# Performance work log

Measured on AMD Instinct MI355X. Metric: run time of the kernel, lower is better.

## Reference

```python
import jax, jax.numpy as jnp
import numpy as np

EPS = 1e-5  # torch LayerNorm default

def layer_norm(x, scale, bias):
    m = jnp.mean(x, axis=-1, keepdims=True)
    v = jnp.var(x, axis=-1, keepdims=True)
    return (x - m) * jax.lax.rsqrt(v + EPS) * scale + bias

def setup_inputs() -> dict:
    key = jax.random.key(0)
    ks = jax.random.split(key, 8)
    B, N, E, D = 2, 50000, 262144, 256
    node_features = jax.random.normal(ks[0], (B, N, D), jnp.float32)
    edge_index = jax.random.randint(ks[1], (B, E, 2), 0, N)
    edge_relations = jax.random.normal(ks[2], (B, E, D), jnp.float32)
    edge_mask = jnp.ones((B, E), jnp.float32)
    sc = 1.0 / np.sqrt(D).astype(np.float32)
    rel_w = jax.random.normal(ks[3], (D, D), jnp.float32) * sc
    rel_b = jnp.zeros((D,), jnp.float32)
    norm_s = jnp.ones((D,), jnp.float32)
    norm_b = jnp.zeros((D,), jnp.float32)
    w1 = jax.random.normal(ks[4], (D, 4 * D), jnp.float32) * sc
    b1 = jnp.zeros((4 * D,), jnp.float32)
    w2 = jax.random.normal(ks[5], (4 * D, D), jnp.float32) * (1.0 / np.sqrt(4 * D).astype(np.float32))
    b2 = jnp.zeros((D,), jnp.float32)
    ffn_s = jnp.ones((D,), jnp.float32)
    ffn_b = jnp.zeros((D,), jnp.float32)
    return dict(node_features=node_features, edge_relations=edge_relations,
                edge_mask=edge_mask, rel_w=rel_w, rel_b=rel_b,
                norm_s=norm_s, norm_b=norm_b, w1=w1, b1=b1, w2=w2, b2=b2,
                ffn_s=ffn_s, ffn_b=ffn_b, edge_index=edge_index)

def reference(node_features, edge_relations, edge_mask, rel_w, rel_b,
              norm_s, norm_b, w1, b1, w2, b2, ffn_s, ffn_b, edge_index):
    B, N, D = node_features.shape
    bidx = jnp.arange(B)[:, None]                      # [B,1] batch index for gather/scatter
    src_idx = edge_index[:, :, 0]                      # [B,E]
    tgt_idx = edge_index[:, :, 1]                      # [B,E]
    src_features = node_features[bidx, src_idx]        # gather -> [B,E,D]
    rel_features = edge_relations @ rel_w + rel_b      # [B,E,D]
    messages = (src_features + rel_features) * edge_mask[..., None]
    aggregated = jnp.zeros_like(node_features).at[bidx, tgt_idx].add(messages)
    counts = jnp.zeros((B, N, 1), node_features.dtype).at[bidx, tgt_idx].add(edge_mask[..., None])
    counts = jnp.maximum(counts, 1.0)
    aggregated = aggregated / counts
    x = layer_norm(node_features + aggregated, norm_s, norm_b)
    h = jax.nn.gelu(x @ w1 + b1, approximate=False)    # torch GELU default = exact erf
    x = layer_norm(x + (h @ w2 + b2), ffn_s, ffn_b)
    return x
```

## Files before the change

kernel.cpp:

```cpp
#include <hip/hip_runtime.h>
#include <math.h>

#define Bn 2
#define Nn 50000
#define En 262144
#define Dn 256
#define Hn 1024
#define RTOT (Bn*Nn)

typedef short bf16x8 __attribute__((ext_vector_type(8)));
typedef float f32x4 __attribute__((ext_vector_type(4)));

__device__ __forceinline__ short f2b(float f) {
  unsigned u = __float_as_uint(f);
  u = u + 0x7fffu + ((u >> 16) & 1u);
  return (short)(u >> 16);
}
__device__ __forceinline__ float b2f(unsigned short s) {
  return __uint_as_float(((unsigned)s) << 16);
}

__device__ __forceinline__ float gelu_f(float v) {
  float x = fabsf(v) * 0.70710678118654752f;
  float t = __builtin_amdgcn_rcpf(1.0f + 0.47047f * x);
  float p = t*(0.3480242f + t*(-0.0958798f + t*0.7478556f));
  float er = 1.0f - p * __expf(-x*x);
  er = copysignf(er, v);
  return 0.5f * v * (1.0f + er);
}

__device__ __forceinline__ void gl16(const void* g, void* l) {
  __builtin_amdgcn_global_load_lds(
      (const __attribute__((address_space(1))) unsigned int*)g,
      (__attribute__((address_space(3))) unsigned int*)l, 16, 0, 0);
}

__global__ void __launch_bounds__(256) wconv(
    const float* __restrict__ relw, const float* __restrict__ w1,
    const float* __restrict__ w2, short* __restrict__ relwT,
    short* __restrict__ w1s, short* __restrict__ w2s) {
  int tid = blockIdx.x * 256 + threadIdx.x;
  if (tid < Dn*Dn) { int c = tid >> 8, k = tid & 255; relwT[tid] = f2b(relw[k*Dn + c]); }
  int t1 = tid - Dn*Dn;
  if (t1 >= 0 && t1 < Dn*Hn) {
    int kk = t1 >> 16, rem = t1 & 65535;
    int col = rem >> 6, kl = rem & 63;
    w1s[kk*65536 + col*64 + (kl ^ ((col & 7) << 3))] = f2b(w1[(kk*64 + kl)*Hn + col]);
  }
  int t2 = tid - Dn*Dn - Dn*Hn;
  if (t2 >= 0 && t2 < Hn*Dn) {
    int kk = t2 >> 14, rem = t2 & 16383;
    int col = rem >> 6, kl = rem & 63;
    w2s[kk*16384 + col*64 + (kl ^ ((col & 7) << 3))] = f2b(w2[(kk*64 + kl)*Dn + col]);
  }
}

__global__ void __launch_bounds__(256) histk(const int* __restrict__ ei, int* __restrict__ cnt) {
  int tid = blockIdx.x * 256 + threadIdx.x;
  if (tid >= Bn*En) return;
  int b = tid / En;
  int tgt = ei[tid*2 + 1];
  atomicAdd(&cnt[b*Nn + tgt], 1);
}

__global__ void __launch_bounds__(256) offsk(const int* __restrict__ cnt,
                                             int* __restrict__ offs, int* __restrict__ gtot) {
  int i = blockIdx.x * 256 + threadIdx.x;
  int lane = threadIdx.x & 63;
  int v = (i < RTOT) ? cnt[i] : 0;
  int s = v;
#pragma unroll
  for (int d = 1; d < 64; d <<= 1) {
    int t = __shfl_up(s, d, 64);
    if (lane >= d) s += t;
  }
  int base = 0;
  if (lane == 63) base = atomicAdd(gtot, s);
  base = __shfl(base, 63, 64);
  if (i < RTOT) offs[i] = base + s - v;
}

__global__ void __launch_bounds__(256) fillk(const int* __restrict__ ei, const int* __restrict__ offs,
                                             int* __restrict__ cursor, int* __restrict__ eids) {
  int tid = blockIdx.x * 256 + threadIdx.x;
  if (tid >= Bn*En) return;
  int b = tid / En, e = tid - b*En;
  int tgt = ei[tid*2 + 1];
  int node = b*Nn + tgt;
  int pos = atomicAdd(&cursor[node], 1);
  eids[offs[node] + pos] = e;
}

__global__ void __launch_bounds__(256) aggk(
    const float* __restrict__ nodef, const float* __restrict__ erel,
    const float* __restrict__ emask, const int* __restrict__ ei,
    const int* __restrict__ offs, const int* __restrict__ cnt,
    const int* __restrict__ eids,
    short* __restrict__ sumrelB, short* __restrict__ sumsrcB, float* __restrict__ cntf) {
  int w = (blockIdx.x * 256 + threadIdx.x) >> 6;
  int lane = threadIdx.x & 63;
  if (w >= RTOT) return;
  int b = w / Nn;
  const size_t ebase = (size_t)b * En;
  const size_t nbase = (size_t)b * Nn;
  int s0 = offs[w], kall = cnt[w];
  int h = lane >> 5, l32 = lane & 31;
  float r[8] = {}, a[8] = {};
  float cf = 0.f;
  for (int base = 0; base < kall; base += 64) {
    int k = kall - base; if (k > 64) k = 64;
    int e = 0, sr = 0; float m = 0.f;
    if (lane < k) {
      e  = eids[s0 + base + lane];
      sr = ei[(ebase + e)*2];
      m  = emask[ebase + e];
    }
    for (int j = 0; j < k; j += 2) {
      int je = j + h;
      int e1  = __shfl(e, je, 64);
      int sr1 = __shfl(sr, je, 64);
      float m1 = __shfl(m, je, 64);
      if (je < k) {
        const float* rp = erel  + (ebase + e1)*Dn + l32*8;
        const float* np = nodef + (nbase + sr1)*Dn + l32*8;
        float4 rv0 = *(const float4*)rp;
        float4 rv1 = *(const float4*)(rp + 4);
        float4 nv0 = *(const float4*)np;
        float4 nv1 = *(const float4*)(np + 4);
        r[0]+=rv0.x*m1; r[1]+=rv0.y*m1; r[2]+=rv0.z*m1; r[3]+=rv0.w*m1;
        r[4]+=rv1.x*m1; r[5]+=rv1.y*m1; r[6]+=rv1.z*m1; r[7]+=rv1.w*m1;
        a[0]+=nv0.x*m1; a[1]+=nv0.y*m1; a[2]+=nv0.z*m1; a[3]+=nv0.w*m1;
        a[4]+=nv1.x*m1; a[5]+=nv1.y*m1; a[6]+=nv1.z*m1; a[7]+=nv1.w*m1;
        cf += m1;
      }
    }
  }
#pragma unroll
  for (int i = 0; i < 8; i++) {
    r[i] += __shfl_xor(r[i], 32, 64);
    a[i] += __shfl_xor(a[i], 32, 64);
  }
  cf += __shfl_xor(cf, 32, 64);
  bf16x8 o;
  if (h == 0) {
#pragma unroll
    for (int i = 0; i < 8; i++) o[i] = f2b(r[i]);
    *(bf16x8*)((char*)sumrelB + (size_t)w*512 + ((l32*16) ^ ((w & 7) << 4))) = o;
  } else {
#pragma unroll
    for (int i = 0; i < 8; i++) o[i] = f2b(a[i]);
    *(bf16x8*)((char*)sumsrcB + (size_t)w*512 + ((l32*16) ^ ((w & 7) << 4))) = o;
  }
  if (lane == 0) cntf[w] = cf;
}

__device__ __forceinline__ bf16x8 ldsA(const char* lds, int r, int kb) {
  int byte = r*512 + (((kb)*2) ^ ((r & 7) << 4));
  return *(const bf16x8*)(lds + byte);
}

__global__ void __launch_bounds__(256, 3) relln(
    const short* __restrict__ sumrelB, const short* __restrict__ relwT,
    const float* __restrict__ relb, const float* __restrict__ nodef,
    const short* __restrict__ sumsrcB, const float* __restrict__ cntf,
    const float* __restrict__ ns, const float* __restrict__ nb,
    short* __restrict__ xb) {
  constexpr int MR = 2;
  __shared__ __align__(16) char lds[16384 + 33280 + 1024];
  char* ldsS = lds;
  char* ldsN = lds + 16384;
  float* red = (float*)(lds + 16384 + 33280);
  int tid = threadIdx.x;
  int lane = tid & 63, wv = tid >> 6;
  int l15 = lane & 15, l4 = lane >> 4;
  int row0 = blockIdx.x * 32;
#pragma unroll
  for (int i = 0; i < 4; i++) {
    int u = tid + 256*i;
    int r = u >> 5, wb = (u & 31) * 16;
    gl16((const char*)sumrelB + (size_t)(row0 + r)*512 + wb, ldsS + u*16);
  }
#pragma unroll
  for (int i = 0; i < 8; i++) {
    int u = tid + 256*i;
    int r = u >> 6, c4 = u & 63;
    float4 v = *(const float4*)(nodef + (size_t)(row0 + r)*Dn + c4*4);
    *(float4*)(ldsN + r*1040 + c4*16) = v;
  }
  __syncthreads();
  f32x4 acc[MR][4] = {};
#pragma unroll
  for (int ks = 0; ks < 8; ks++) {
    bf16x8 af[MR], bfr[4];
#pragma unroll
    for (int m = 0; m < MR; m++) af[m] = ldsA(ldsS, m*16 + l15, ks*32 + l4*8);
#pragma unroll
    for (int n = 0; n < 4; n++) {
      int col = wv*64 + n*16 + l15;
      bfr[n] = *(const bf16x8*)(relwT + col*Dn + ks*32 + l4*8);
    }
#pragma unroll
    for (int m = 0; m < MR; m++)
#pragma unroll
      for (int n = 0; n < 4; n++)
        acc[m][n] = __builtin_amdgcn_mfma_f32_16x16x32_bf16(af[m], bfr[n], acc[m][n], 0, 0, 0);
  }
  __syncthreads();
#pragma unroll
  for (int i = 0; i < 4; i++) {
    int u = tid + 256*i;
    int r = u >> 5, wb = (u & 31) * 16;
    gl16((const char*)sumsrcB + (size_t)(row0 + r)*512 + wb, ldsS + u*16);
  }
  __syncthreads();
  int cols[4]; float rb_c[4], ns_c[4], nb_c[4];
#pragma unroll
  for (int n = 0; n < 4; n++) {
    cols[n] = wv*64 + n*16 + l15;
    rb_c[n] = relb[cols[n]]; ns_c[n] = ns[cols[n]]; nb_c[n] = nb[cols[n]];
  }
  float s1[MR][4], s2[MR][4];
#pragma unroll
  for (int m = 0; m < MR; m++)
#pragma unroll
    for (int g = 0; g < 4; g++) {
      int r = m*16 + l4*4 + g; int rg = row0 + r;
      float cf  = cntf[rg];
      float inv = 1.0f / fmaxf(cf, 1.0f);
      float aa = 0.f, qq = 0.f;
#pragma unroll
      for (int n = 0; n < 4; n++) {
        float ssrc = b2f(*(const unsigned short*)(ldsS + r*512 + ((cols[n]*2) ^ ((r & 7) << 4))));
        float nfv  = *(const float*)(ldsN + r*1040 + cols[n]*4);
        float vv = nfv + (ssrc + acc[m][n][g] + cf*rb_c[n]) * inv;
        acc[m][n][g] = vv;
        aa += vv; qq += vv*vv;
      }
#pragma unroll
      for (int d = 1; d < 16; d <<= 1) { aa += __shfl_xor(aa, d, 16); qq += __shfl_xor(qq, d, 16); }
      s1[m][g] = aa; s2[m][g] = qq;
    }
  if (l15 == 0) {
#pragma unroll
    for (int m = 0; m < MR; m++)
#pragma unroll
      for (int g = 0; g < 4; g++) {
        int r = m*16 + l4*4 + g;
        red[(wv*32 + r)*2]     = s1[m][g];
        red[(wv*32 + r)*2 + 1] = s2[m][g];
      }
  }
  __syncthreads();
#pragma unroll
  for (int m = 0; m < MR; m++)
#pragma unroll
    for (int g = 0; g < 4; g++) {
      int r = m*16 + l4*4 + g; int rg = row0 + r;
      float t1 = 0.f, t2 = 0.f;
#pragma unroll
      for (int u = 0; u < 4; u++) { t1 += red[(u*32 + r)*2]; t2 += red[(u*32 + r)*2 + 1]; }
      float mean = t1 * (1.0f/Dn);
      float var  = t2 * (1.0f/Dn) - mean*mean;
      float rstd = rsqrtf(var + 1e-5f);
#pragma unroll
      for (int n = 0; n < 4; n++) {
        float xv = (acc[m][n][g] - mean)*rstd*ns_c[n] + nb_c[n];
        *(short*)((char*)xb + (size_t)rg*512 + ((cols[n]*2) ^ ((rg & 7) << 4))) = f2b(xv);
      }
    }
}

__global__ void __launch_bounds__(256) ffn1k(
    const short* __restrict__ xb, const short* __restrict__ w1s,
    const float* __restrict__ b1, short* __restrict__ H) {
  __shared__ __align__(16) char lds[32768];
  char* Xa = lds;
  char* Wa = lds + 16384;
  int tid = threadIdx.x;
  int lane = tid & 63, wv = tid >> 6;
  int l15 = lane & 15, l4 = lane >> 4;
  int wm = wv >> 1, wn = wv & 1;
  int row0 = blockIdx.x * 128;
  int col0 = blockIdx.y * 128;

  f32x4 acc[4][4] = {};
#pragma unroll 1
  for (int kk = 0; kk < 4; kk++) {
#pragma unroll
    for (int i = 0; i < 4; i++) {
      int u = tid + 256*i;
      int r = u >> 3, wb = (u & 7) * 16;
      int gr = row0 + r; if (gr > RTOT - 1) gr = RTOT - 1;
      gl16((const char*)xb + (size_t)gr*512 + kk*128 + wb, Xa + u*16);
    }
#pragma unroll
    for (int i = 0; i < 4; i++) {
      int u = tid + 256*i;
      gl16((const char*)w1s + (size_t)kk*131072 + col0*128 + u*16, Wa + u*16);
    }
    __syncthreads();
#pragma unroll
    for (int ksl = 0; ksl < 2; ksl++) {
      int kb2 = (ksl*32 + l4*8) * 2;
      bf16x8 af[4], bw[4];
#pragma unroll
      for (int mf = 0; mf < 4; mf++) {
        int r = wm*64 + mf*16 + l15;
        af[mf] = *(const bf16x8*)(Xa + r*128 + (kb2 ^ ((r & 7) << 4)));
      }
#pragma unroll
      for (int nf = 0; nf < 4; nf++) {
        int c = wn*64 + nf*16 + l15;
        bw[nf] = *(const bf16x8*)(Wa + c*128 + (kb2 ^ ((c & 7) << 4)));
      }
#pragma unroll
      for (int mf = 0; mf < 4; mf++)
#pragma unroll
        for (int nf = 0; nf < 4; nf++)
          acc[mf][nf] = __builtin_amdgcn_mfma_f32_16x16x32_bf16(af[mf], bw[nf], acc[mf][nf], 0, 0, 0);
    }
    __syncthreads();
  }
  float b1v[4];
#pragma unroll
  for (int nf = 0; nf < 4; nf++) b1v[nf] = b1[col0 + wn*64 + nf*16 + l15];
#pragma unroll
  for (int mf = 0; mf < 4; mf++)
#pragma unroll
    for (int g = 0; g < 4; g++) {
      int R = wm*64 + mf*16 + l4*4 + g;
#pragma unroll
      for (int nf = 0; nf < 4; nf++) {
        int C = wn*64 + nf*16 + l15;
        float hv = gelu_f(acc[mf][nf][g] + b1v[nf]);
        *(short*)(lds + R*256 + ((C*2) ^ ((R & 7) << 4))) = f2b(hv);
      }
    }
  __syncthreads();
#pragma unroll
  for (int i = 0; i < 8; i++) {
    int u = tid + 256*i;
    int r = u >> 4, c = (u & 15) * 8;
    int gr = row0 + r;
    if (gr >= RTOT) continue;
    bf16x8 v = *(const bf16x8*)(lds + r*256 + ((c*2) ^ ((r & 7) << 4)));
    int gc = col0 + c;
    size_t hb = (size_t)gr*2048 + (gc >> 6)*128 + (((gc & 63)*2) ^ ((gr & 7) << 4));
    *(bf16x8*)((char*)H + hb) = v;
  }
}

__global__ void __launch_bounds__(512, 4) ffn2k(
    const short* __restrict__ H, const short* __restrict__ w2s,
    const float* __restrict__ b2, const float* __restrict__ fs,
    const float* __restrict__ fb, const short* __restrict__ xb,
    float* __restrict__ out) {
  __shared__ __align__(16) char lds[8192 + 32768];
  char* Ha  = lds;
  char* W2a = lds + 8192;
  float* red = (float*)lds;
  int tid = threadIdx.x;
  int lane = tid & 63, wv = tid >> 6;
  int l15 = lane & 15, l4 = lane >> 4;
  int wm = wv >> 2, wn = wv & 3;
  int rows0 = blockIdx.x * 64;

  f32x4 acc[2][4] = {};
#pragma unroll 1
  for (int kk = 0; kk < 16; kk++) {
    {
      int flat = wv*1024 + lane*16;
      int r = flat >> 7, bo = flat & 127;
      int lr = rows0 + r; if (lr > RTOT - 1) lr = RTOT - 1;
      gl16((const char*)H + (size_t)lr*2048 + kk*128 + bo, Ha + flat);
    }
#pragma unroll
    for (int i = 0; i < 4; i++) {
      int base = wv*4096 + i*1024;
      gl16((const char*)w2s + (size_t)kk*32768 + base + lane*16, W2a + base + lane*16);
    }
    __syncthreads();
#pragma unroll
    for (int ksl = 0; ksl < 2; ksl++) {
      bf16x8 ah[2], bw[4];
#pragma unroll
      for (int mf = 0; mf < 2; mf++) {
        int r = wm*32 + mf*16 + l15;
        ah[mf] = *(const bf16x8*)(Ha + r*128 + (((ksl*32 + l4*8)*2) ^ ((r & 7) << 4)));
      }
#pragma unroll
      for (int nf = 0; nf < 4; nf++) {
        int c = wn*64 + nf*16 + l15;
        bw[nf] = *(const bf16x8*)(W2a + c*128 + (((ksl*32 + l4*8)*2) ^ ((c & 7) << 4)));
      }
#pragma unroll
      for (int mf = 0; mf < 2; mf++)
#pragma unroll
        for (int nf = 0; nf < 4; nf++)
          acc[mf][nf] = __builtin_amdgcn_mfma_f32_16x16x32_bf16(ah[mf], bw[nf], acc[mf][nf], 0, 0, 0);
    }
    __syncthreads();
  }
#pragma unroll
  for (int i = 0; i < 4; i++) {
    int u = tid + 512*i;
    int r = u >> 5, wb = (u & 31) * 16;
    int lr = rows0 + r; if (lr > RTOT - 1) lr = RTOT - 1;
    gl16((const char*)xb + (size_t)lr*512 + wb, W2a + u*16);
  }
  __syncthreads();
  float b2c[4], fsc[4], fbc[4];
#pragma unroll
  for (int nf = 0; nf < 4; nf++) {
    int col = wn*64 + nf*16 + l15;
    b2c[nf] = b2[col]; fsc[nf] = fs[col]; fbc[nf] = fb[col];
  }
#pragma unroll
  for (int mf = 0; mf < 2; mf++)
#pragma unroll
    for (int g = 0; g < 4; g++) {
      int R = wm*32 + mf*16 + l4*4 + g;
      float a = 0.f, q = 0.f;
#pragma unroll
      for (int nf = 0; nf < 4; nf++) {
        int col = wn*64 + nf*16 + l15;
        float xv = b2f(*(const unsigned short*)(W2a + R*512 + ((col*2) ^ ((R & 7) << 4))));
        float vv = xv + acc[mf][nf][g] + b2c[nf];
        acc[mf][nf][g] = vv;
        a += vv; q += vv*vv;
      }
#pragma unroll
      for (int d = 1; d < 16; d <<= 1) { a += __shfl_xor(a, d, 16); q += __shfl_xor(q, d, 16); }
      if (l15 == 0) {
        red[(wn*64 + R)*2]     = a;
        red[(wn*64 + R)*2 + 1] = q;
      }
    }
  __syncthreads();
#pragma unroll
  for (int mf = 0; mf < 2; mf++)
#pragma unroll
    for (int g = 0; g < 4; g++) {
      int R = wm*32 + mf*16 + l4*4 + g;
      int gr = rows0 + R;
      if (gr >= RTOT) continue;
      float t1 = 0.f, t2 = 0.f;
#pragma unroll
      for (int u = 0; u < 4; u++) { t1 += red[(u*64 + R)*2]; t2 += red[(u*64 + R)*2 + 1]; }
      float mean = t1 * (1.0f/Dn);
      float var  = t2 * (1.0f/Dn) - mean*mean;
      float rstd = rsqrtf(var + 1e-5f);
#pragma unroll
      for (int nf = 0; nf < 4; nf++) {
        int col = wn*64 + nf*16 + l15;
        out[(size_t)gr*Dn + col] = (acc[mf][nf][g] - mean)*rstd*fsc[nf] + fbc[nf];
      }
    }
}

extern "C" void kernel_launch(void* const* d_in, const int* in_sizes, int n_in,
                              void* d_out, int out_size, void* d_ws, size_t ws_size,
                              hipStream_t stream) {
  const float* nodef = (const float*)d_in[0];
  const float* erel  = (const float*)d_in[1];
  const float* emask = (const float*)d_in[2];
  const float* relw  = (const float*)d_in[3];
  const float* relb  = (const float*)d_in[4];
  const float* ns    = (const float*)d_in[5];
  const float* nb    = (const float*)d_in[6];
  const float* w1    = (const float*)d_in[7];
  const float* b1    = (const float*)d_in[8];
  const float* w2    = (const float*)d_in[9];
  const float* b2    = (const float*)d_in[10];
  const float* fs    = (const float*)d_in[11];
  const float* fb    = (const float*)d_in[12];
  const int*   ei    = (const int*)d_in[13];
  float* out = (float*)d_out;
  char* ws = (char*)d_ws;

  constexpr size_t SZ_ROWB = (size_t)RTOT * Dn * 2;
  constexpr size_t O_SRB = 0;
  constexpr size_t O_SSB = O_SRB + SZ_ROWB;
  constexpr size_t O_XB  = O_SSB + SZ_ROWB;
  constexpr size_t O_H   = O_XB + SZ_ROWB;
  constexpr size_t O_CNT = O_H + (size_t)RTOT * Hn * 2;
  constexpr size_t O_CUR = O_CNT + (size_t)RTOT*4;
  constexpr size_t O_OFF = O_CUR + (size_t)RTOT*4;
  constexpr size_t O_EID = O_OFF + ((size_t)(RTOT+1)*4 + 124);
  constexpr size_t O_CNTF = O_EID + (size_t)Bn*En*4;
  constexpr size_t O_RWT = O_CNTF + (size_t)RTOT*4;
  constexpr size_t O_W1T = O_RWT + (size_t)Dn*Dn*2;
  constexpr size_t O_W2T = O_W1T + (size_t)Dn*Hn*2;
  constexpr size_t WS_NEED = O_W2T + (size_t)Hn*Dn*2;
  if (ws_size < WS_NEED) return;

  short* sumrelB = (short*)(ws + O_SRB);
  short* sumsrcB = (short*)(ws + O_SSB);
  short* xb      = (short*)(ws + O_XB);
  short* Hbuf    = (short*)(ws + O_H);
  int*   cnt    = (int*)(ws + O_CNT);
  int*   cursor = (int*)(ws + O_CUR);
  int*   offs   = (int*)(ws + O_OFF);
  int*   eids   = (int*)(ws + O_EID);
  float* cntf   = (float*)(ws + O_CNTF);
  short* relwT  = (short*)(ws + O_RWT);
  short* w1s    = (short*)(ws + O_W1T);
  short* w2s    = (short*)(ws + O_W2T);
  int*   gtot   = offs + RTOT;

  hipMemsetAsync(ws + O_CNT, 0, O_EID - O_CNT, stream);

  wconv<<<(Dn*Dn + Dn*Hn + Hn*Dn + 255) / 256, 256, 0, stream>>>(relw, w1, w2, relwT, w1s, w2s);
  histk<<<(Bn*En) / 256, 256, 0, stream>>>(ei, cnt);
  offsk<<<(RTOT + 255) / 256, 256, 0, stream>>>(cnt, offs, gtot);
  fillk<<<(Bn*En) / 256, 256, 0, stream>>>(ei, offs, cursor, eids);
  aggk<<<(RTOT + 3) / 4, 256, 0, stream>>>(nodef, erel, emask, ei, offs, cnt, eids,
                                           sumrelB, sumsrcB, cntf);
  relln<<<RTOT / 32, 256, 0, stream>>>(sumrelB, relwT, relb, nodef, sumsrcB, cntf, ns, nb, xb);
  ffn1k<<<dim3((RTOT + 127) / 128, Hn / 128), 256, 0, stream>>>(xb, w1s, b1, Hbuf);
  ffn2k<<<(RTOT + 63) / 64, 512, 0, stream>>>(Hbuf, w2s, b2, fs, fb, xb, out);
}
```

Before: 612.1 us.

## Pack edge records in CSR fill and widen per-edge gather to four edges per wave

```diff
diff --git a/kernel.cpp b/kernel.cpp
--- a/kernel.cpp
+++ b/kernel.cpp
@@ -80,22 +80,23 @@
   if (i < RTOT) offs[i] = base + s - v;
 }
 
-__global__ void __launch_bounds__(256) fillk(const int* __restrict__ ei, const int* __restrict__ offs,
-                                             int* __restrict__ cursor, int* __restrict__ eids) {
+__global__ void __launch_bounds__(256) fillk(const int* __restrict__ ei,
+                                             const float* __restrict__ emask,
+                                             int* __restrict__ offs, int4* __restrict__ erec) {
   int tid = blockIdx.x * 256 + threadIdx.x;
   if (tid >= Bn*En) return;
   int b = tid / En, e = tid - b*En;
-  int tgt = ei[tid*2 + 1];
-  int node = b*Nn + tgt;
-  int pos = atomicAdd(&cursor[node], 1);
-  eids[offs[node] + pos] = e;
+  int2 st = *(const int2*)(ei + (size_t)tid*2);
+  float m = emask[tid];
+  int node = b*Nn + st.y;
+  int pos = atomicAdd(&offs[node], 1);
+  erec[pos] = make_int4(e, st.x, __float_as_int(m), 0);
 }
 
 __global__ void __launch_bounds__(256) aggk(
     const float* __restrict__ nodef, const float* __restrict__ erel,
-    const float* __restrict__ emask, const int* __restrict__ ei,
     const int* __restrict__ offs, const int* __restrict__ cnt,
-    const int* __restrict__ eids,
+    const int4* __restrict__ erec,
     short* __restrict__ sumrelB, short* __restrict__ sumsrcB, float* __restrict__ cntf) {
   int w = (blockIdx.x * 256 + threadIdx.x) >> 6;
   int lane = threadIdx.x & 63;
@@ -103,53 +104,56 @@
   int b = w / Nn;
   const size_t ebase = (size_t)b * En;
   const size_t nbase = (size_t)b * Nn;
-  int s0 = offs[w], kall = cnt[w];
-  int h = lane >> 5, l32 = lane & 31;
-  float r[8] = {}, a[8] = {};
+  int kall = cnt[w];
+  int s0 = offs[w] - kall;
+  int g = lane >> 4, l16 = lane & 15;
+  float r[16] = {}, a[16] = {};
   float cf = 0.f;
   for (int base = 0; base < kall; base += 64) {
     int k = kall - base; if (k > 64) k = 64;
-    int e = 0, sr = 0; float m = 0.f;
-    if (lane < k) {
-      e  = eids[s0 + base + lane];
-      sr = ei[(ebase + e)*2];
-      m  = emask[ebase + e];
-    }
-    for (int j = 0; j < k; j += 2) {
-      int je = j + h;
-      int e1  = __shfl(e, je, 64);
-      int sr1 = __shfl(sr, je, 64);
-      float m1 = __shfl(m, je, 64);
+    int4 rec = make_int4(0, 0, 0, 0);
+    if (lane < k) rec = erec[s0 + base + lane];
+    for (int j = 0; j < k; j += 4) {
+      int je = j + g;
+      int e1  = __shfl(rec.x, je, 64);
+      int sr1 = __shfl(rec.y, je, 64);
+      float m1 = __int_as_float(__shfl(rec.z, je, 64));
       if (je < k) {
-        const float* rp = erel  + (ebase + e1)*Dn + l32*8;
-        const float* np = nodef + (nbase + sr1)*Dn + l32*8;
-        float4 rv0 = *(const float4*)rp;
-        float4 rv1 = *(const float4*)(rp + 4);
-        float4 nv0 = *(const float4*)np;
-        float4 nv1 = *(const float4*)(np + 4);
-        r[0]+=rv0.x*m1; r[1]+=rv0.y*m1; r[2]+=rv0.z*m1; r[3]+=rv0.w*m1;
-        r[4]+=rv1.x*m1; r[5]+=rv1.y*m1; r[6]+=rv1.z*m1; r[7]+=rv1.w*m1;
-        a[0]+=nv0.x*m1; a[1]+=nv0.y*m1; a[2]+=nv0.z*m1; a[3]+=nv0.w*m1;
-        a[4]+=nv1.x*m1; a[5]+=nv1.y*m1; a[6]+=nv1.z*m1; a[7]+=nv1.w*m1;
+        const float* rp = erel  + (ebase + e1)*Dn + l16*16;
+        const float* np = nodef + (nbase + sr1)*Dn + l16*16;
+#pragma unroll
+        for (int q = 0; q < 4; q++) {
+          float4 rv = *(const float4*)(rp + q*4);
+          float4 nv = *(const float4*)(np + q*4);
+          r[q*4+0]+=rv.x*m1; r[q*4+1]+=rv.y*m1; r[q*4+2]+=rv.z*m1; r[q*4+3]+=rv.w*m1;
+          a[q*4+0]+=nv.x*m1; a[q*4+1]+=nv.y*m1; a[q*4+2]+=nv.z*m1; a[q*4+3]+=nv.w*m1;
+        }
         cf += m1;
       }
     }
   }
 #pragma unroll
-  for (int i = 0; i < 8; i++) {
+  for (int i = 0; i < 16; i++) {
+    r[i] += __shfl_xor(r[i], 16, 64);
+    a[i] += __shfl_xor(a[i], 16, 64);
     r[i] += __shfl_xor(r[i], 32, 64);
     a[i] += __shfl_xor(a[i], 32, 64);
   }
+  cf += __shfl_xor(cf, 16, 64);
   cf += __shfl_xor(cf, 32, 64);
-  bf16x8 o;
-  if (h == 0) {
-#pragma unroll
-    for (int i = 0; i < 8; i++) o[i] = f2b(r[i]);
-    *(bf16x8*)((char*)sumrelB + (size_t)w*512 + ((l32*16) ^ ((w & 7) << 4))) = o;
-  } else {
-#pragma unroll
-    for (int i = 0; i < 8; i++) o[i] = f2b(a[i]);
-    *(bf16x8*)((char*)sumsrcB + (size_t)w*512 + ((l32*16) ^ ((w & 7) << 4))) = o;
+  int c0 = l16*32;
+  if (g == 0) {
+    bf16x8 o0, o1;
+#pragma unroll
+    for (int i = 0; i < 8; i++) { o0[i] = f2b(r[i]); o1[i] = f2b(r[i+8]); }
+    *(bf16x8*)((char*)sumrelB + (size_t)w*512 + (c0 ^ ((w & 7) << 4))) = o0;
+    *(bf16x8*)((char*)sumrelB + (size_t)w*512 + ((c0+16) ^ ((w & 7) << 4))) = o1;
+  } else if (g == 1) {
+    bf16x8 o0, o1;
+#pragma unroll
+    for (int i = 0; i < 8; i++) { o0[i] = f2b(a[i]); o1[i] = f2b(a[i+8]); }
+    *(bf16x8*)((char*)sumsrcB + (size_t)w*512 + (c0 ^ ((w & 7) << 4))) = o0;
+    *(bf16x8*)((char*)sumsrcB + (size_t)w*512 + ((c0+16) ^ ((w & 7) << 4))) = o1;
   }
   if (lane == 0) cntf[w] = cf;
 }
@@ -484,10 +488,10 @@
   constexpr size_t O_XB  = O_SSB + SZ_ROWB;
   constexpr size_t O_H   = O_XB + SZ_ROWB;
   constexpr size_t O_CNT = O_H + (size_t)RTOT * Hn * 2;
-  constexpr size_t O_CUR = O_CNT + (size_t)RTOT*4;
-  constexpr size_t O_OFF = O_CUR + (size_t)RTOT*4;
-  constexpr size_t O_EID = O_OFF + ((size_t)(RTOT+1)*4 + 124);
-  constexpr size_t O_CNTF = O_EID + (size_t)Bn*En*4;
+  constexpr size_t O_GT  = O_CNT + (size_t)RTOT*4;
+  constexpr size_t O_OFF = O_GT + 128;
+  constexpr size_t O_REC = O_OFF + (size_t)RTOT*4 + 112;
+  constexpr size_t O_CNTF = O_REC + (size_t)Bn*En*16;
   constexpr size_t O_RWT = O_CNTF + (size_t)RTOT*4;
   constexpr size_t O_W1T = O_RWT + (size_t)Dn*Dn*2;
   constexpr size_t O_W2T = O_W1T + (size_t)Dn*Hn*2;
@@ -499,22 +503,21 @@
   short* xb      = (short*)(ws + O_XB);
   short* Hbuf    = (short*)(ws + O_H);
   int*   cnt    = (int*)(ws + O_CNT);
-  int*   cursor = (int*)(ws + O_CUR);
+  int*   gtot   = (int*)(ws + O_GT);
   int*   offs   = (int*)(ws + O_OFF);
-  int*   eids   = (int*)(ws + O_EID);
+  int4*  erec   = (int4*)(ws + O_REC);
   float* cntf   = (float*)(ws + O_CNTF);
   short* relwT  = (short*)(ws + O_RWT);
   short* w1s    = (short*)(ws + O_W1T);
   short* w2s    = (short*)(ws + O_W2T);
-  int*   gtot   = offs + RTOT;
-
-  hipMemsetAsync(ws + O_CNT, 0, O_EID - O_CNT, stream);
+
+  hipMemsetAsync(ws + O_CNT, 0, (size_t)RTOT*4 + 128, stream);
 
   wconv<<<(Dn*Dn + Dn*Hn + Hn*Dn + 255) / 256, 256, 0, stream>>>(relw, w1, w2, relwT, w1s, w2s);
   histk<<<(Bn*En) / 256, 256, 0, stream>>>(ei, cnt);
   offsk<<<(RTOT + 255) / 256, 256, 0, stream>>>(cnt, offs, gtot);
-  fillk<<<(Bn*En) / 256, 256, 0, stream>>>(ei, offs, cursor, eids);
-  aggk<<<(RTOT + 3) / 4, 256, 0, stream>>>(nodef, erel, emask, ei, offs, cnt, eids,
+  fillk<<<(Bn*En) / 256, 256, 0, stream>>>(ei, emask, offs, erec);
+  aggk<<<(RTOT + 3) / 4, 256, 0, stream>>>(nodef, erel, offs, cnt, erec,
                                            sumrelB, sumsrcB, cntf);
   relln<<<RTOT / 32, 256, 0, stream>>>(sumrelB, relwT, relb, nodef, sumsrcB, cntf, ns, nb, xb);
   ffn1k<<<dim3((RTOT + 127) / 128, Hn / 128), 256, 0, stream>>>(xb, w1s, b1, Hbuf);
```

Result: no change. 612.7 us (+0.1%).
